# Kernel tuning notes

Hardware: AMD Instinct MI355X
Metric: run time of the kernel (lower is better)

The kernel has to match this reference:

```python
import jax, jax.numpy as jnp
import numpy as np

TEMPERATURE = 0.07
EPS = 1e-8  # torch CosineSimilarity norm clamp

N, D, NUM_CLASSES = 4096, 768, 128


def setup_inputs() -> dict:
    key = jax.random.key(0)
    k1, k2, k3 = jax.random.split(key, 3)
    img_emb = jax.random.normal(k1, (N, D), dtype=jnp.float32)
    text_emb = jax.random.normal(k2, (N, D), dtype=jnp.float32)
    labels = jax.random.randint(k3, (N,), 0, NUM_CLASSES, dtype=jnp.int64)
    return {"img_emb": img_emb, "text_emb": text_emb, "labels": labels}


def reference(img_emb, text_emb, labels):
    # cosine similarity via normalize + matmul (avoids O(N^2 D) broadcast)
    img_n = img_emb / jnp.maximum(jnp.linalg.norm(img_emb, axis=-1, keepdims=True), EPS)
    txt_n = text_emb / jnp.maximum(jnp.linalg.norm(text_emb, axis=-1, keepdims=True), EPS)
    logits = jnp.einsum('id,jd->ij', img_n, txt_n) / TEMPERATURE  # [N, N]

    pos_mask = (labels[:, None] == labels[None, :]).astype(logits.dtype)  # [N, N]

    img2text = -(pos_mask * jax.nn.log_softmax(logits, axis=1)).sum(1).mean()
    text2img = -(pos_mask * jax.nn.log_softmax(logits, axis=0)).sum(0).mean()
    return (img2text + text2img) / 2
```

## Files before the change

kernel.cpp:

```cpp
#include <hip/hip_runtime.h>
#include <hip/hip_bf16.h>

#define N_ 4096
#define D_ 768
#define NCLS 128
#define BM 128
#define BN 128
#define BK 64
#define NSTEP 12

typedef __bf16 bf16x8 __attribute__((ext_vector_type(8)));
typedef float f32x4 __attribute__((ext_vector_type(4)));

#define SBAR() asm volatile("s_barrier" ::: "memory")
#define VMWAIT8() asm volatile("s_waitcnt vmcnt(8)" ::: "memory")
#define LGKM0() asm volatile("s_waitcnt lgkmcnt(0)" ::: "memory")

__device__ __forceinline__ void gload16(const unsigned short* g, unsigned short* l) {
  __builtin_amdgcn_global_load_lds(
      (const __attribute__((address_space(1))) unsigned int*)g,
      (__attribute__((address_space(3))) unsigned int*)l, 16, 0, 0);
}

__global__ __launch_bounds__(192) void normalize_kernel(
    const float* __restrict__ img, const float* __restrict__ txt,
    __hip_bfloat16* __restrict__ img_nb, __hip_bfloat16* __restrict__ txt_nb,
    double* __restrict__ accs, unsigned* __restrict__ cnt) {
  int b = blockIdx.x;
  if (b == 0 && threadIdx.x == 0) {
    accs[0] = 0.0;
    accs[1] = 0.0;
    *cnt = 0u;
  }
  const float* s;
  __hip_bfloat16* d;
  if (b < N_) {
    s = img + (size_t)b * D_;
    d = img_nb + (size_t)b * D_;
  } else {
    s = txt + (size_t)(b - N_) * D_;
    d = txt_nb + (size_t)(b - N_) * D_;
  }
  int tid = threadIdx.x;
  float4 v = ((const float4*)s)[tid];
  float ss = v.x * v.x + v.y * v.y + v.z * v.z + v.w * v.w;
#pragma unroll
  for (int m = 32; m; m >>= 1) ss += __shfl_xor(ss, m);
  __shared__ float wsum[3];
  int lane = tid & 63, w = tid >> 6;
  if (lane == 0) wsum[w] = ss;
  __syncthreads();
  float inv = 1.0f / fmaxf(sqrtf(wsum[0] + wsum[1] + wsum[2]), 1e-8f);
  ushort4 o;
  o.x = __bfloat16_as_ushort(__float2bfloat16(v.x * inv));
  o.y = __bfloat16_as_ushort(__float2bfloat16(v.y * inv));
  o.z = __bfloat16_as_ushort(__float2bfloat16(v.z * inv));
  o.w = __bfloat16_as_ushort(__float2bfloat16(v.w * inv));
  ((ushort4*)d)[tid] = o;
}

__global__ __launch_bounds__(256) void gemm_epi_kernel(
    const unsigned short* __restrict__ A, const unsigned short* __restrict__ B,
    const int* __restrict__ labels, float* __restrict__ row_part,
    float* __restrict__ col_part, float* __restrict__ S_part) {
  __shared__ __align__(16) unsigned short As[2][8192];
  __shared__ __align__(16) unsigned short Bs[2][8192];
  __shared__ int labR[BM], labC[BN];
  __shared__ float rbuf[2][BM], cbuf[2][BN];
  __shared__ float sbuf[4];

  const int lin = blockIdx.y * 32 + blockIdx.x;
  const int xcd = lin & 7, idx = lin >> 3;
  const int bx = xcd * 4 + (idx & 3), by = idx >> 2;

  const int tid = threadIdx.x;
  const int lane = tid & 63, wave = tid >> 6;
  const int wr = wave >> 1, wc = wave & 1;
  const int g = lane >> 4, fr = lane & 15;
  const int rowBase = by * BM, colBase = bx * BN;

  if (tid < BM) labR[tid] = labels[rowBase + tid];
  else labC[tid - BM] = labels[colBase + tid - BM];
  __syncthreads();

  const int r0 = lane >> 3;
  const int cswz = (lane & 7) ^ (r0 & 7);
  const unsigned short* pa = A + (size_t)(rowBase + wave * 8 + r0) * D_ + cswz * 8;
  const unsigned short* pb = B + (size_t)(colBase + wave * 8 + r0) * D_ + cswz * 8;
  const int dbase = wave * 8 * 64;

#pragma unroll
  for (int j = 0; j < 4; ++j) {
    gload16(pa + (size_t)(32 * j) * D_, &As[0][dbase + j * 2048]);
    gload16(pb + (size_t)(32 * j) * D_, &Bs[0][dbase + j * 2048]);
  }

  f32x4 acc[4][4] = {};

  for (int u = 0; u < NSTEP; ++u) {
    SBAR();
    {
      const int su = (u + 1 < NSTEP) ? u + 1 : u;
      const size_t kk = (size_t)su * BK;
      const int sl = (u + 1) & 1;
#pragma unroll
      for (int j = 0; j < 4; ++j) {
        gload16(pa + (size_t)(32 * j) * D_ + kk, &As[sl][dbase + j * 2048]);
        gload16(pb + (size_t)(32 * j) * D_ + kk, &Bs[sl][dbase + j * 2048]);
      }
    }
    VMWAIT8();
    SBAR();
    const unsigned short* as_ = As[u & 1];
    const unsigned short* bs_ = Bs[u & 1];
#pragma unroll
    for (int ks = 0; ks < 2; ++ks) {
      const int sw = (ks * 4 + g) ^ (fr & 7);
      bf16x8 af[4], bf[4];
#pragma unroll
      for (int m = 0; m < 4; ++m)
        af[m] = *(const bf16x8*)&as_[((wr * 64 + m * 16 + fr) * 8 + sw) * 8];
#pragma unroll
      for (int n = 0; n < 4; ++n)
        bf[n] = *(const bf16x8*)&bs_[((wc * 64 + n * 16 + fr) * 8 + sw) * 8];
#pragma unroll
      for (int m = 0; m < 4; ++m)
#pragma unroll
        for (int n = 0; n < 4; ++n)
          acc[m][n] = __builtin_amdgcn_mfma_f32_16x16x32_bf16(af[m], bf[n], acc[m][n], 0, 0, 0);
    }
    LGKM0();
  }
  __syncthreads();

  const float scale = 14.285714285714286f;
  float sPart = 0.f;
  float colAcc[4] = {0.f, 0.f, 0.f, 0.f};
#pragma unroll
  for (int m = 0; m < 4; ++m) {
    float ra2[4] = {0.f, 0.f, 0.f, 0.f};
#pragma unroll
    for (int n = 0; n < 4; ++n) {
      int col = wc * 64 + n * 16 + fr;
      int lc = labC[col];
#pragma unroll
      for (int r = 0; r < 4; ++r) {
        float v = acc[m][n][r] * scale;
        float e = __expf(v);
        ra2[r] += e;
        colAcc[n] += e;
        int row = wr * 64 + m * 16 + g * 4 + r;
        if (labR[row] == lc) sPart += v;
      }
    }
#pragma unroll
    for (int r = 0; r < 4; ++r) {
      float x = ra2[r];
      x += __shfl_xor(x, 1);
      x += __shfl_xor(x, 2);
      x += __shfl_xor(x, 4);
      x += __shfl_xor(x, 8);
      if (fr == 0) rbuf[wc][wr * 64 + m * 16 + g * 4 + r] = x;
    }
  }
#pragma unroll
  for (int n = 0; n < 4; ++n) {
    float x = colAcc[n];
    x += __shfl_xor(x, 16);
    x += __shfl_xor(x, 32);
    if (g == 0) cbuf[wr][wc * 64 + n * 16 + fr] = x;
  }
  float s = sPart;
#pragma unroll
  for (int m = 32; m; m >>= 1) s += __shfl_xor(s, m);
  if (lane == 0) sbuf[wave] = s;
  __syncthreads();
  if (tid < BM)
    row_part[(size_t)bx * N_ + rowBase + tid] = rbuf[0][tid] + rbuf[1][tid];
  else
    col_part[(size_t)by * N_ + colBase + (tid - BM)] = cbuf[0][tid - BM] + cbuf[1][tid - BM];
  if (tid == 0) S_part[by * 32 + bx] = sbuf[0] + sbuf[1] + sbuf[2] + sbuf[3];
}

__global__ __launch_bounds__(256) void reduce_kernel(
    const float* __restrict__ row_part, const float* __restrict__ col_part,
    const float* __restrict__ S_part, const int* __restrict__ labels,
    double* __restrict__ accs, unsigned* __restrict__ cnt, float* __restrict__ out) {
  __shared__ int hist[NCLS];
  int tid = threadIdx.x;
  if (tid < NCLS) hist[tid] = 0;
  __syncthreads();
  for (int j = tid; j < N_; j += 256) atomicAdd(&hist[labels[j]], 1);
  __syncthreads();

  int i = blockIdx.x * 256 + tid;
  float rs = 0.f, cs = 0.f;
#pragma unroll
  for (int b = 0; b < 32; ++b) {
    rs += row_part[(size_t)b * N_ + i];
    cs += col_part[(size_t)b * N_ + i];
  }
  int c = hist[labels[i]];
  double term = (double)c * ((double)logf(rs) + (double)logf(cs));
  double sterm = (i < 1024) ? (double)S_part[i] : 0.0;
#pragma unroll
  for (int m = 32; m; m >>= 1) {
    term += __shfl_xor(term, m);
    sterm += __shfl_xor(sterm, m);
  }
  __shared__ double tbuf[4], sb[4];
  int lane = tid & 63, w = tid >> 6;
  if (lane == 0) { tbuf[w] = term; sb[w] = sterm; }
  __syncthreads();
  if (tid == 0) {
    atomicAdd(&accs[0], tbuf[0] + tbuf[1] + tbuf[2] + tbuf[3]);
    atomicAdd(&accs[1], sb[0] + sb[1] + sb[2] + sb[3]);
    __threadfence();
    unsigned old = atomicAdd(cnt, 1u);
    if (old == 15u) {
      double t = atomicAdd(&accs[0], 0.0);
      double s2 = atomicAdd(&accs[1], 0.0);
      out[0] = (float)((t - 2.0 * s2) / (2.0 * (double)N_));
    }
  }
}

extern "C" void kernel_launch(void* const* d_in, const int* in_sizes, int n_in,
                              void* d_out, int out_size, void* d_ws, size_t ws_size,
                              hipStream_t stream) {
  const float* img = (const float*)d_in[0];
  const float* txt = (const float*)d_in[1];
  const int* labels = (const int*)d_in[2];
  float* out = (float*)d_out;
  char* ws = (char*)d_ws;

  __hip_bfloat16* img_nb = (__hip_bfloat16*)(ws);
  __hip_bfloat16* txt_nb = (__hip_bfloat16*)(ws + 6291456);
  float* row_part = (float*)(ws + 12582912);
  float* col_part = (float*)(ws + 13107200);
  float* S_part = (float*)(ws + 13631488);
  double* accs = (double*)(ws + 13635584);
  unsigned* cnt = (unsigned*)(ws + 13635600);

  normalize_kernel<<<2 * N_, 192, 0, stream>>>(img, txt, img_nb, txt_nb, accs, cnt);
  gemm_epi_kernel<<<dim3(32, 32), 256, 0, stream>>>(
      (const unsigned short*)img_nb, (const unsigned short*)txt_nb, labels,
      row_part, col_part, S_part);
  reduce_kernel<<<16, 256, 0, stream>>>(row_part, col_part, S_part, labels, accs, cnt, out);
}
```

Before: 53.91 us.

## Double GEMM row tile to 256 so each wave computes 128x64

Grows the GEMM block tile from 128x128 to 256x128. Each wave now holds an 8x4 grid of MFMA accumulators, which raises reuse of the B fragments and halves the number of blocks to 512. The LDS A buffer doubles in size, the vmcnt wait is adjusted to the new load count, and the epilogue and reduce kernel are updated for 16 row blocks. In exchange, register pressure and LDS use per block rise, which may lower occupancy, and fewer blocks means less parallelism across the CUs.

```diff
diff --git a/kernel.cpp b/kernel.cpp
--- a/kernel.cpp
+++ b/kernel.cpp
@@ -4,7 +4,7 @@
 #define N_ 4096
 #define D_ 768
 #define NCLS 128
-#define BM 128
+#define BM 256
 #define BN 128
 #define BK 64
 #define NSTEP 12
@@ -13,7 +13,7 @@
 typedef float f32x4 __attribute__((ext_vector_type(4)));
 
 #define SBAR() asm volatile("s_barrier" ::: "memory")
-#define VMWAIT8() asm volatile("s_waitcnt vmcnt(8)" ::: "memory")
+#define VMWAIT12() asm volatile("s_waitcnt vmcnt(12)" ::: "memory")
 #define LGKM0() asm volatile("s_waitcnt lgkmcnt(0)" ::: "memory")
 
 __device__ __forceinline__ void gload16(const unsigned short* g, unsigned short* l) {
@@ -63,7 +63,7 @@
     const unsigned short* __restrict__ A, const unsigned short* __restrict__ B,
     const int* __restrict__ labels, float* __restrict__ row_part,
     float* __restrict__ col_part, float* __restrict__ S_part) {
-  __shared__ __align__(16) unsigned short As[2][8192];
+  __shared__ __align__(16) unsigned short As[2][16384];
   __shared__ __align__(16) unsigned short Bs[2][8192];
   __shared__ int labR[BM], labC[BN];
   __shared__ float rbuf[2][BM], cbuf[2][BN];
@@ -79,23 +79,24 @@
   const int g = lane >> 4, fr = lane & 15;
   const int rowBase = by * BM, colBase = bx * BN;
 
-  if (tid < BM) labR[tid] = labels[rowBase + tid];
-  else labC[tid - BM] = labels[colBase + tid - BM];
+  labR[tid] = labels[rowBase + tid];
+  if (tid < BN) labC[tid] = labels[colBase + tid];
   __syncthreads();
 
   const int r0 = lane >> 3;
   const int cswz = (lane & 7) ^ (r0 & 7);
   const unsigned short* pa = A + (size_t)(rowBase + wave * 8 + r0) * D_ + cswz * 8;
   const unsigned short* pb = B + (size_t)(colBase + wave * 8 + r0) * D_ + cswz * 8;
-  const int dbase = wave * 8 * 64;
-
-#pragma unroll
-  for (int j = 0; j < 4; ++j) {
+  const int dbase = wave * 512;
+
+#pragma unroll
+  for (int j = 0; j < 8; ++j)
     gload16(pa + (size_t)(32 * j) * D_, &As[0][dbase + j * 2048]);
+#pragma unroll
+  for (int j = 0; j < 4; ++j)
     gload16(pb + (size_t)(32 * j) * D_, &Bs[0][dbase + j * 2048]);
-  }
-
-  f32x4 acc[4][4] = {};
+
+  f32x4 acc[8][4] = {};
 
   for (int u = 0; u < NSTEP; ++u) {
     SBAR();
@@ -104,30 +105,30 @@
       const size_t kk = (size_t)su * BK;
       const int sl = (u + 1) & 1;
 #pragma unroll
-      for (int j = 0; j < 4; ++j) {
+      for (int j = 0; j < 8; ++j)
         gload16(pa + (size_t)(32 * j) * D_ + kk, &As[sl][dbase + j * 2048]);
+#pragma unroll
+      for (int j = 0; j < 4; ++j)
         gload16(pb + (size_t)(32 * j) * D_ + kk, &Bs[sl][dbase + j * 2048]);
-      }
-    }
-    VMWAIT8();
+    }
+    VMWAIT12();
     SBAR();
     const unsigned short* as_ = As[u & 1];
     const unsigned short* bs_ = Bs[u & 1];
 #pragma unroll
     for (int ks = 0; ks < 2; ++ks) {
       const int sw = (ks * 4 + g) ^ (fr & 7);
-      bf16x8 af[4], bf[4];
-#pragma unroll
-      for (int m = 0; m < 4; ++m)
-        af[m] = *(const bf16x8*)&as_[((wr * 64 + m * 16 + fr) * 8 + sw) * 8];
+      bf16x8 bf[4];
 #pragma unroll
       for (int n = 0; n < 4; ++n)
         bf[n] = *(const bf16x8*)&bs_[((wc * 64 + n * 16 + fr) * 8 + sw) * 8];
 #pragma unroll
-      for (int m = 0; m < 4; ++m)
+      for (int m = 0; m < 8; ++m) {
+        bf16x8 af = *(const bf16x8*)&as_[((wr * 128 + m * 16 + fr) * 8 + sw) * 8];
 #pragma unroll
         for (int n = 0; n < 4; ++n)
-          acc[m][n] = __builtin_amdgcn_mfma_f32_16x16x32_bf16(af[m], bf[n], acc[m][n], 0, 0, 0);
+          acc[m][n] = __builtin_amdgcn_mfma_f32_16x16x32_bf16(af, bf[n], acc[m][n], 0, 0, 0);
+      }
     }
     LGKM0();
   }
@@ -137,7 +138,7 @@
   float sPart = 0.f;
   float colAcc[4] = {0.f, 0.f, 0.f, 0.f};
 #pragma unroll
-  for (int m = 0; m < 4; ++m) {
+  for (int m = 0; m < 8; ++m) {
     float ra2[4] = {0.f, 0.f, 0.f, 0.f};
 #pragma unroll
     for (int n = 0; n < 4; ++n) {
@@ -149,7 +150,7 @@
         float e = __expf(v);
         ra2[r] += e;
         colAcc[n] += e;
-        int row = wr * 64 + m * 16 + g * 4 + r;
+        int row = wr * 128 + m * 16 + g * 4 + r;
         if (labR[row] == lc) sPart += v;
       }
     }
@@ -160,7 +161,7 @@
       x += __shfl_xor(x, 2);
       x += __shfl_xor(x, 4);
       x += __shfl_xor(x, 8);
-      if (fr == 0) rbuf[wc][wr * 64 + m * 16 + g * 4 + r] = x;
+      if (fr == 0) rbuf[wc][wr * 128 + m * 16 + g * 4 + r] = x;
     }
   }
 #pragma unroll
@@ -168,18 +169,18 @@
     float x = colAcc[n];
     x += __shfl_xor(x, 16);
     x += __shfl_xor(x, 32);
-    if (g == 0) cbuf[wr][wc * 64 + n * 16 + fr] = x;
+    if (lane < 16) cbuf[wr][wc * 64 + n * 16 + fr] = x;
   }
   float s = sPart;
 #pragma unroll
   for (int m = 32; m; m >>= 1) s += __shfl_xor(s, m);
   if (lane == 0) sbuf[wave] = s;
   __syncthreads();
-  if (tid < BM)
-    row_part[(size_t)bx * N_ + rowBase + tid] = rbuf[0][tid] + rbuf[1][tid];
-  else
-    col_part[(size_t)by * N_ + colBase + (tid - BM)] = cbuf[0][tid - BM] + cbuf[1][tid - BM];
-  if (tid == 0) S_part[by * 32 + bx] = sbuf[0] + sbuf[1] + sbuf[2] + sbuf[3];
+  row_part[(size_t)bx * N_ + rowBase + tid] = rbuf[0][tid] + rbuf[1][tid];
+  if (tid < BN)
+    col_part[(size_t)by * N_ + colBase + tid] = cbuf[0][tid] + cbuf[1][tid];
+  if (tid == 0)
+    S_part[by * 32 + bx] = sbuf[0] + sbuf[1] + sbuf[2] + sbuf[3];
 }
 
 __global__ __launch_bounds__(256) void reduce_kernel(
@@ -196,13 +197,12 @@
   int i = blockIdx.x * 256 + tid;
   float rs = 0.f, cs = 0.f;
 #pragma unroll
-  for (int b = 0; b < 32; ++b) {
-    rs += row_part[(size_t)b * N_ + i];
-    cs += col_part[(size_t)b * N_ + i];
-  }
+  for (int b = 0; b < 32; ++b) rs += row_part[(size_t)b * N_ + i];
+#pragma unroll
+  for (int b = 0; b < 16; ++b) cs += col_part[(size_t)b * N_ + i];
   int c = hist[labels[i]];
   double term = (double)c * ((double)logf(rs) + (double)logf(cs));
-  double sterm = (i < 1024) ? (double)S_part[i] : 0.0;
+  double sterm = (i < 512) ? (double)S_part[i] : 0.0;
 #pragma unroll
   for (int m = 32; m; m >>= 1) {
     term += __shfl_xor(term, m);
@@ -238,12 +238,12 @@
   __hip_bfloat16* txt_nb = (__hip_bfloat16*)(ws + 6291456);
   float* row_part = (float*)(ws + 12582912);
   float* col_part = (float*)(ws + 13107200);
-  float* S_part = (float*)(ws + 13631488);
-  double* accs = (double*)(ws + 13635584);
-  unsigned* cnt = (unsigned*)(ws + 13635600);
+  float* S_part = (float*)(ws + 13369344);
+  double* accs = (double*)(ws + 13371392);
+  unsigned* cnt = (unsigned*)(ws + 13371408);
 
   normalize_kernel<<<2 * N_, 192, 0, stream>>>(img, txt, img_nb, txt_nb, accs, cnt);
-  gemm_epi_kernel<<<dim3(32, 32), 256, 0, stream>>>(
+  gemm_epi_kernel<<<dim3(32, 16), 256, 0, stream>>>(
       (const unsigned short*)img_nb, (const unsigned short*)txt_nb, labels,
       row_part, col_part, S_part);
   reduce_kernel<<<16, 256, 0, stream>>>(row_part, col_part, S_part, labels, accs, cnt, out);
```

Result: slower. 77.32 us (+43.4%).

## Use 8 waves per GEMM tile with BK=32 and a shallower LDS pipeline

Applied to the files above, without the earlier changes.

The GEMM block grows from 4 to 8 waves, so each wave now computes a 64x32 sub-tile instead of 64x64. The K step is halved to 32, which halves LDS per block, and each thread issues one async global-to-LDS load per operand per step. The swizzle and the epilogue reductions are adapted to match. The aim is more waves per CU to hide latency, at the cost of twice as many barrier-synchronised K iterations and less MFMA work per barrier.

```diff
diff --git a/kernel.cpp b/kernel.cpp
--- a/kernel.cpp
+++ b/kernel.cpp
@@ -6,14 +6,14 @@
 #define NCLS 128
 #define BM 128
 #define BN 128
-#define BK 64
-#define NSTEP 12
+#define BK 32
+#define NSTEP 24
 
 typedef __bf16 bf16x8 __attribute__((ext_vector_type(8)));
 typedef float f32x4 __attribute__((ext_vector_type(4)));
 
 #define SBAR() asm volatile("s_barrier" ::: "memory")
-#define VMWAIT8() asm volatile("s_waitcnt vmcnt(8)" ::: "memory")
+#define VMWAIT2() asm volatile("s_waitcnt vmcnt(2)" ::: "memory")
 #define LGKM0() asm volatile("s_waitcnt lgkmcnt(0)" ::: "memory")
 
 __device__ __forceinline__ void gload16(const unsigned short* g, unsigned short* l) {
@@ -59,15 +59,15 @@
   ((ushort4*)d)[tid] = o;
 }
 
-__global__ __launch_bounds__(256) void gemm_epi_kernel(
+__global__ __launch_bounds__(512) void gemm_epi_kernel(
     const unsigned short* __restrict__ A, const unsigned short* __restrict__ B,
     const int* __restrict__ labels, float* __restrict__ row_part,
     float* __restrict__ col_part, float* __restrict__ S_part) {
-  __shared__ __align__(16) unsigned short As[2][8192];
-  __shared__ __align__(16) unsigned short Bs[2][8192];
+  __shared__ __align__(16) unsigned short As[2][4096];
+  __shared__ __align__(16) unsigned short Bs[2][4096];
   __shared__ int labR[BM], labC[BN];
-  __shared__ float rbuf[2][BM], cbuf[2][BN];
-  __shared__ float sbuf[4];
+  __shared__ float rbuf[4][BM], cbuf[2][BN];
+  __shared__ float sbuf[8];
 
   const int lin = blockIdx.y * 32 + blockIdx.x;
   const int xcd = lin & 7, idx = lin >> 3;
@@ -75,27 +75,24 @@
 
   const int tid = threadIdx.x;
   const int lane = tid & 63, wave = tid >> 6;
-  const int wr = wave >> 1, wc = wave & 1;
+  const int wr = wave >> 2, wc = wave & 3;
   const int g = lane >> 4, fr = lane & 15;
   const int rowBase = by * BM, colBase = bx * BN;
 
   if (tid < BM) labR[tid] = labels[rowBase + tid];
-  else labC[tid - BM] = labels[colBase + tid - BM];
-  __syncthreads();
-
-  const int r0 = lane >> 3;
-  const int cswz = (lane & 7) ^ (r0 & 7);
-  const unsigned short* pa = A + (size_t)(rowBase + wave * 8 + r0) * D_ + cswz * 8;
-  const unsigned short* pb = B + (size_t)(colBase + wave * 8 + r0) * D_ + cswz * 8;
-  const int dbase = wave * 8 * 64;
-
-#pragma unroll
-  for (int j = 0; j < 4; ++j) {
-    gload16(pa + (size_t)(32 * j) * D_, &As[0][dbase + j * 2048]);
-    gload16(pb + (size_t)(32 * j) * D_, &Bs[0][dbase + j * 2048]);
-  }
-
-  f32x4 acc[4][4] = {};
+  else if (tid < BM + BN) labC[tid - BM] = labels[colBase + tid - BM];
+  __syncthreads();
+
+  const int srow = tid >> 2;
+  const int cswz = (tid & 3) ^ ((srow >> 1) & 3);
+  const unsigned short* pa = A + (size_t)(rowBase + srow) * D_ + cswz * 8;
+  const unsigned short* pb = B + (size_t)(colBase + srow) * D_ + cswz * 8;
+  const int dpos = (wave * 64) * 8;
+
+  gload16(pa, &As[0][dpos]);
+  gload16(pb, &Bs[0][dpos]);
+
+  f32x4 acc[4][2] = {};
 
   for (int u = 0; u < NSTEP; ++u) {
     SBAR();
@@ -103,45 +100,39 @@
       const int su = (u + 1 < NSTEP) ? u + 1 : u;
       const size_t kk = (size_t)su * BK;
       const int sl = (u + 1) & 1;
-#pragma unroll
-      for (int j = 0; j < 4; ++j) {
-        gload16(pa + (size_t)(32 * j) * D_ + kk, &As[sl][dbase + j * 2048]);
-        gload16(pb + (size_t)(32 * j) * D_ + kk, &Bs[sl][dbase + j * 2048]);
-      }
-    }
-    VMWAIT8();
+      gload16(pa + kk, &As[sl][dpos]);
+      gload16(pb + kk, &Bs[sl][dpos]);
+    }
+    VMWAIT2();
     SBAR();
     const unsigned short* as_ = As[u & 1];
     const unsigned short* bs_ = Bs[u & 1];
-#pragma unroll
-    for (int ks = 0; ks < 2; ++ks) {
-      const int sw = (ks * 4 + g) ^ (fr & 7);
-      bf16x8 af[4], bf[4];
-#pragma unroll
-      for (int m = 0; m < 4; ++m)
-        af[m] = *(const bf16x8*)&as_[((wr * 64 + m * 16 + fr) * 8 + sw) * 8];
-#pragma unroll
-      for (int n = 0; n < 4; ++n)
-        bf[n] = *(const bf16x8*)&bs_[((wc * 64 + n * 16 + fr) * 8 + sw) * 8];
-#pragma unroll
-      for (int m = 0; m < 4; ++m)
-#pragma unroll
-        for (int n = 0; n < 4; ++n)
-          acc[m][n] = __builtin_amdgcn_mfma_f32_16x16x32_bf16(af[m], bf[n], acc[m][n], 0, 0, 0);
-    }
+    const int sw = g ^ ((fr >> 1) & 3);
+    bf16x8 af[4], bf[2];
+#pragma unroll
+    for (int m = 0; m < 4; ++m)
+      af[m] = *(const bf16x8*)&as_[((wr * 64 + m * 16 + fr) * 4 + sw) * 8];
+#pragma unroll
+    for (int n = 0; n < 2; ++n)
+      bf[n] = *(const bf16x8*)&bs_[((wc * 32 + n * 16 + fr) * 4 + sw) * 8];
+#pragma unroll
+    for (int m = 0; m < 4; ++m)
+#pragma unroll
+      for (int n = 0; n < 2; ++n)
+        acc[m][n] = __builtin_amdgcn_mfma_f32_16x16x32_bf16(af[m], bf[n], acc[m][n], 0, 0, 0);
     LGKM0();
   }
   __syncthreads();
 
   const float scale = 14.285714285714286f;
   float sPart = 0.f;
-  float colAcc[4] = {0.f, 0.f, 0.f, 0.f};
+  float colAcc[2] = {0.f, 0.f};
 #pragma unroll
   for (int m = 0; m < 4; ++m) {
     float ra2[4] = {0.f, 0.f, 0.f, 0.f};
 #pragma unroll
-    for (int n = 0; n < 4; ++n) {
-      int col = wc * 64 + n * 16 + fr;
+    for (int n = 0; n < 2; ++n) {
+      int col = wc * 32 + n * 16 + fr;
       int lc = labC[col];
 #pragma unroll
       for (int r = 0; r < 4; ++r) {
@@ -164,11 +155,11 @@
     }
   }
 #pragma unroll
-  for (int n = 0; n < 4; ++n) {
+  for (int n = 0; n < 2; ++n) {
     float x = colAcc[n];
     x += __shfl_xor(x, 16);
     x += __shfl_xor(x, 32);
-    if (g == 0) cbuf[wr][wc * 64 + n * 16 + fr] = x;
+    if (g == 0) cbuf[wr][wc * 32 + n * 16 + fr] = x;
   }
   float s = sPart;
 #pragma unroll
@@ -176,10 +167,15 @@
   if (lane == 0) sbuf[wave] = s;
   __syncthreads();
   if (tid < BM)
-    row_part[(size_t)bx * N_ + rowBase + tid] = rbuf[0][tid] + rbuf[1][tid];
-  else
-    col_part[(size_t)by * N_ + colBase + (tid - BM)] = cbuf[0][tid - BM] + cbuf[1][tid - BM];
-  if (tid == 0) S_part[by * 32 + bx] = sbuf[0] + sbuf[1] + sbuf[2] + sbuf[3];
+    row_part[(size_t)bx * N_ + rowBase + tid] =
+        rbuf[0][tid] + rbuf[1][tid] + rbuf[2][tid] + rbuf[3][tid];
+  else if (tid < BM + BN) {
+    int c = tid - BM;
+    col_part[(size_t)by * N_ + colBase + c] = cbuf[0][c] + cbuf[1][c];
+  }
+  if (tid == 0)
+    S_part[by * 32 + bx] =
+        sbuf[0] + sbuf[1] + sbuf[2] + sbuf[3] + sbuf[4] + sbuf[5] + sbuf[6] + sbuf[7];
 }
 
 __global__ __launch_bounds__(256) void reduce_kernel(
@@ -243,7 +239,7 @@
   unsigned* cnt = (unsigned*)(ws + 13635600);
 
   normalize_kernel<<<2 * N_, 192, 0, stream>>>(img, txt, img_nb, txt_nb, accs, cnt);
-  gemm_epi_kernel<<<dim3(32, 32), 256, 0, stream>>>(
+  gemm_epi_kernel<<<dim3(32, 32), 512, 0, stream>>>(
       (const unsigned short*)img_nb, (const unsigned short*)txt_nb, labels,
       row_part, col_part, S_part);
   reduce_kernel<<<16, 256, 0, stream>>>(row_part, col_part, S_part, labels, accs, cnt, out);
```

Result: slower. 59.73 us (+10.8%).

## Switch normalized embeddings and GEMM from bf16 to fp8 MFMA

Applied to the files above, without the earlier changes.

The normalize kernel now writes FP8 (e4m3) values instead of bf16, using a permuted k layout within each 128-byte segment so that each lane's 16-byte LDS load feeds two 16x16x32 fp8 MFMAs. The GEMM tile is reworked for byte-sized elements: BK doubles to 128 bytes per step, six steps, and the shared-memory layout changes to match. This halves the memory traffic and uses the higher-throughput fp8 MFMA path. In exchange, logits lose precision, which is scaled by 1/T=14.3 before exp and could push the loss past tolerance.

```diff
diff --git a/kernel.cpp b/kernel.cpp
--- a/kernel.cpp
+++ b/kernel.cpp
@@ -6,17 +6,17 @@
 #define NCLS 128
 #define BM 128
 #define BN 128
-#define BK 64
-#define NSTEP 12
-
-typedef __bf16 bf16x8 __attribute__((ext_vector_type(8)));
+#define BKB 128
+#define NSTEP 6
+
 typedef float f32x4 __attribute__((ext_vector_type(4)));
+typedef long lng2 __attribute__((ext_vector_type(2)));
 
 #define SBAR() asm volatile("s_barrier" ::: "memory")
 #define VMWAIT8() asm volatile("s_waitcnt vmcnt(8)" ::: "memory")
 #define LGKM0() asm volatile("s_waitcnt lgkmcnt(0)" ::: "memory")
 
-__device__ __forceinline__ void gload16(const unsigned short* g, unsigned short* l) {
+__device__ __forceinline__ void gload16(const unsigned char* g, unsigned char* l) {
   __builtin_amdgcn_global_load_lds(
       (const __attribute__((address_space(1))) unsigned int*)g,
       (__attribute__((address_space(3))) unsigned int*)l, 16, 0, 0);
@@ -24,7 +24,7 @@
 
 __global__ __launch_bounds__(192) void normalize_kernel(
     const float* __restrict__ img, const float* __restrict__ txt,
-    __hip_bfloat16* __restrict__ img_nb, __hip_bfloat16* __restrict__ txt_nb,
+    unsigned char* __restrict__ img_f8, unsigned char* __restrict__ txt_f8,
     double* __restrict__ accs, unsigned* __restrict__ cnt) {
   int b = blockIdx.x;
   if (b == 0 && threadIdx.x == 0) {
@@ -33,13 +33,13 @@
     *cnt = 0u;
   }
   const float* s;
-  __hip_bfloat16* d;
+  unsigned char* d;
   if (b < N_) {
     s = img + (size_t)b * D_;
-    d = img_nb + (size_t)b * D_;
+    d = img_f8 + (size_t)b * D_;
   } else {
     s = txt + (size_t)(b - N_) * D_;
-    d = txt_nb + (size_t)(b - N_) * D_;
+    d = txt_f8 + (size_t)(b - N_) * D_;
   }
   int tid = threadIdx.x;
   float4 v = ((const float4*)s)[tid];
@@ -51,20 +51,21 @@
   if (lane == 0) wsum[w] = ss;
   __syncthreads();
   float inv = 1.0f / fmaxf(sqrtf(wsum[0] + wsum[1] + wsum[2]), 1e-8f);
-  ushort4 o;
-  o.x = __bfloat16_as_ushort(__float2bfloat16(v.x * inv));
-  o.y = __bfloat16_as_ushort(__float2bfloat16(v.y * inv));
-  o.z = __bfloat16_as_ushort(__float2bfloat16(v.z * inv));
-  o.w = __bfloat16_as_ushort(__float2bfloat16(v.w * inv));
-  ((ushort4*)d)[tid] = o;
+  int r = 0;
+  r = __builtin_amdgcn_cvt_pk_fp8_f32(v.x * inv, v.y * inv, r, false);
+  r = __builtin_amdgcn_cvt_pk_fp8_f32(v.z * inv, v.w * inv, r, true);
+  const int k0 = tid * 4;
+  const int seg = k0 >> 7, ko = k0 & 127;
+  const int ks = ko >> 5, gg = (ko >> 3) & 3, h = (ko >> 2) & 1;
+  ((int*)d)[seg * 32 + (gg * 2 + (ks >> 1)) * 4 + (ks & 1) * 2 + h] = r;
 }
 
 __global__ __launch_bounds__(256) void gemm_epi_kernel(
-    const unsigned short* __restrict__ A, const unsigned short* __restrict__ B,
+    const unsigned char* __restrict__ A, const unsigned char* __restrict__ B,
     const int* __restrict__ labels, float* __restrict__ row_part,
     float* __restrict__ col_part, float* __restrict__ S_part) {
-  __shared__ __align__(16) unsigned short As[2][8192];
-  __shared__ __align__(16) unsigned short Bs[2][8192];
+  __shared__ __align__(16) unsigned char As[2][16384];
+  __shared__ __align__(16) unsigned char Bs[2][16384];
   __shared__ int labR[BM], labC[BN];
   __shared__ float rbuf[2][BM], cbuf[2][BN];
   __shared__ float sbuf[4];
@@ -85,14 +86,14 @@
 
   const int r0 = lane >> 3;
   const int cswz = (lane & 7) ^ (r0 & 7);
-  const unsigned short* pa = A + (size_t)(rowBase + wave * 8 + r0) * D_ + cswz * 8;
-  const unsigned short* pb = B + (size_t)(colBase + wave * 8 + r0) * D_ + cswz * 8;
-  const int dbase = wave * 8 * 64;
+  const unsigned char* pa = A + (size_t)(rowBase + wave * 8 + r0) * D_ + cswz * 16;
+  const unsigned char* pb = B + (size_t)(colBase + wave * 8 + r0) * D_ + cswz * 16;
+  const int dbase = wave * 1024;
 
 #pragma unroll
   for (int j = 0; j < 4; ++j) {
-    gload16(pa + (size_t)(32 * j) * D_, &As[0][dbase + j * 2048]);
-    gload16(pb + (size_t)(32 * j) * D_, &Bs[0][dbase + j * 2048]);
+    gload16(pa + (size_t)(32 * j) * D_, &As[0][dbase + j * 4096]);
+    gload16(pb + (size_t)(32 * j) * D_, &Bs[0][dbase + j * 4096]);
   }
 
   f32x4 acc[4][4] = {};
@@ -101,33 +102,37 @@
     SBAR();
     {
       const int su = (u + 1 < NSTEP) ? u + 1 : u;
-      const size_t kk = (size_t)su * BK;
+      const size_t kk = (size_t)su * BKB;
       const int sl = (u + 1) & 1;
 #pragma unroll
       for (int j = 0; j < 4; ++j) {
-        gload16(pa + (size_t)(32 * j) * D_ + kk, &As[sl][dbase + j * 2048]);
-        gload16(pb + (size_t)(32 * j) * D_ + kk, &Bs[sl][dbase + j * 2048]);
+        gload16(pa + (size_t)(32 * j) * D_ + kk, &As[sl][dbase + j * 4096]);
+        gload16(pb + (size_t)(32 * j) * D_ + kk, &Bs[sl][dbase + j * 4096]);
       }
     }
     VMWAIT8();
     SBAR();
-    const unsigned short* as_ = As[u & 1];
-    const unsigned short* bs_ = Bs[u & 1];
-#pragma unroll
-    for (int ks = 0; ks < 2; ++ks) {
-      const int sw = (ks * 4 + g) ^ (fr & 7);
-      bf16x8 af[4], bf[4];
-#pragma unroll
-      for (int m = 0; m < 4; ++m)
-        af[m] = *(const bf16x8*)&as_[((wr * 64 + m * 16 + fr) * 8 + sw) * 8];
-#pragma unroll
-      for (int n = 0; n < 4; ++n)
-        bf[n] = *(const bf16x8*)&bs_[((wc * 64 + n * 16 + fr) * 8 + sw) * 8];
-#pragma unroll
-      for (int m = 0; m < 4; ++m)
-#pragma unroll
-        for (int n = 0; n < 4; ++n)
-          acc[m][n] = __builtin_amdgcn_mfma_f32_16x16x32_bf16(af[m], bf[n], acc[m][n], 0, 0, 0);
+    const unsigned char* as_ = As[u & 1];
+    const unsigned char* bs_ = Bs[u & 1];
+#pragma unroll
+    for (int p = 0; p < 2; ++p) {
+      const int gp = g * 2 + p;
+      lng2 bq[4];
+#pragma unroll
+      for (int n = 0; n < 4; ++n) {
+        const int row = wc * 64 + n * 16 + fr;
+        bq[n] = *(const lng2*)&bs_[row * 128 + (gp ^ (fr & 7)) * 16];
+      }
+#pragma unroll
+      for (int m = 0; m < 4; ++m) {
+        const int row = wr * 64 + m * 16 + fr;
+        lng2 aq = *(const lng2*)&as_[row * 128 + (gp ^ (fr & 7)) * 16];
+#pragma unroll
+        for (int n = 0; n < 4; ++n) {
+          acc[m][n] = __builtin_amdgcn_mfma_f32_16x16x32_fp8_fp8(aq[0], bq[n][0], acc[m][n], 0, 0, 0);
+          acc[m][n] = __builtin_amdgcn_mfma_f32_16x16x32_fp8_fp8(aq[1], bq[n][1], acc[m][n], 0, 0, 0);
+        }
+      }
     }
     LGKM0();
   }
@@ -234,17 +239,16 @@
   float* out = (float*)d_out;
   char* ws = (char*)d_ws;
 
-  __hip_bfloat16* img_nb = (__hip_bfloat16*)(ws);
-  __hip_bfloat16* txt_nb = (__hip_bfloat16*)(ws + 6291456);
-  float* row_part = (float*)(ws + 12582912);
-  float* col_part = (float*)(ws + 13107200);
-  float* S_part = (float*)(ws + 13631488);
-  double* accs = (double*)(ws + 13635584);
-  unsigned* cnt = (unsigned*)(ws + 13635600);
-
-  normalize_kernel<<<2 * N_, 192, 0, stream>>>(img, txt, img_nb, txt_nb, accs, cnt);
+  unsigned char* img_f8 = (unsigned char*)(ws);
+  unsigned char* txt_f8 = (unsigned char*)(ws + 3145728);
+  float* row_part = (float*)(ws + 6291456);
+  float* col_part = (float*)(ws + 6815744);
+  float* S_part = (float*)(ws + 7340032);
+  double* accs = (double*)(ws + 7344128);
+  unsigned* cnt = (unsigned*)(ws + 7344144);
+
+  normalize_kernel<<<2 * N_, 192, 0, stream>>>(img, txt, img_f8, txt_f8, accs, cnt);
   gemm_epi_kernel<<<dim3(32, 32), 256, 0, stream>>>(
-      (const unsigned short*)img_nb, (const unsigned short*)txt_nb, labels,
-      row_part, col_part, S_part);
+      img_f8, txt_f8, labels, row_part, col_part, S_part);
   reduce_kernel<<<16, 256, 0, stream>>>(row_part, col_part, S_part, labels, accs, cnt, out);
 }
```

Result: faster. 46.19 us (-14.3%).
